# Optimization experiments

Hardware: AMD Instinct MI355X
Metric: run time of the kernel (lower is better)

Reference implementation:

```python
import jax, jax.numpy as jnp
import numpy as np

DIM = 768
HEAD = 12


def setup_inputs() -> dict:
    key = jax.random.key(0)
    ks = jax.random.split(key, 7)
    B, N, C = 4, 2048, DIM
    s = 0.02
    return {
        "x": jax.random.normal(ks[0], (B, N, C), dtype=jnp.float32),
        "wq": jax.random.normal(ks[1], (C, C), dtype=jnp.float32) * s,
        "bq": jax.random.normal(ks[2], (C,), dtype=jnp.float32) * s,
        "wkv": jax.random.normal(ks[3], (C, 2 * C), dtype=jnp.float32) * s,
        "bkv": jax.random.normal(ks[4], (2 * C,), dtype=jnp.float32) * s,
        "wp": jax.random.normal(ks[5], (C, C), dtype=jnp.float32) * s,
        "bp": jax.random.normal(ks[6], (C,), dtype=jnp.float32) * s,
    }


def reference(x, wq, bq, wkv, bkv, wp, bp):
    B, N, C = x.shape
    H = HEAD
    D = C // H
    scale = D ** -0.5
    # projections
    q = (x @ wq + bq).reshape(B, N, H, D)          # [B,N,H,D]
    kv = (x @ wkv + bkv).reshape(B, N, 2, H, D)
    k = kv[:, :, 0]                                 # [B,N,H,D]
    v = kv[:, :, 1]
    # attention scores [B,H,N,N]
    attn = jnp.einsum('bnhd,bmhd->bhnm', q, k) * scale
    attn = jax.nn.softmax(attn, axis=-1)
    x_atten = jnp.einsum('bhnm,bmhd->bnhd', attn, v).reshape(B, N, C)
    return x_atten @ wp + bp
```

## Files before the change

kernel.cpp:

```cpp
#include <hip/hip_runtime.h>

typedef unsigned short u16;
typedef __attribute__((ext_vector_type(8))) short bf16x8;
typedef __attribute__((ext_vector_type(4))) float f32x4;

#define MFMA(a, b, c) __builtin_amdgcn_mfma_f32_16x16x32_bf16(a, b, c, 0, 0, 0)
#define LOG2E 1.44269504088896340736f

__device__ __forceinline__ u16 f2bf(float f) {
    union { float f; unsigned u; } v; v.f = f;
    unsigned r = v.u + 0x7fffu + ((v.u >> 16) & 1u);
    return (u16)(r >> 16);
}
__device__ __forceinline__ float bf2f(u16 h) {
    union { unsigned u; float f; } v; v.u = ((unsigned)h) << 16;
    return v.f;
}
__device__ __forceinline__ unsigned pkbf(float a, float b) {
#if __has_builtin(__builtin_amdgcn_cvt_pk_bf16_f32)
    typedef __attribute__((ext_vector_type(2))) __bf16 bf2_t;
    bf2_t v = __builtin_amdgcn_cvt_pk_bf16_f32(a, b);
    return __builtin_bit_cast(unsigned, v);
#else
    return (unsigned)f2bf(a) | ((unsigned)f2bf(b) << 16);
#endif
}
__device__ __forceinline__ float ex2(float x) {
#if __has_builtin(__builtin_amdgcn_exp2f)
    return __builtin_amdgcn_exp2f(x);
#else
    return exp2f(x);
#endif
}
__device__ __forceinline__ bf16x8 frag_from(unsigned a, unsigned b, unsigned c, unsigned d) {
    uint4 v; v.x = a; v.y = b; v.z = c; v.w = d;
    return __builtin_bit_cast(bf16x8, v);
}

__device__ __forceinline__ void g2l16(const void* g, void* lds_base) {
    __builtin_amdgcn_global_load_lds(
        (const __attribute__((address_space(1))) unsigned*)(unsigned long long)(uintptr_t)g,
        (__attribute__((address_space(3))) unsigned*)(unsigned)(uintptr_t)lds_base,
        16, 0, 0);
}

__global__ __launch_bounds__(256) void prep_kernel(
    const float* __restrict__ x, const float* __restrict__ wq,
    const float* __restrict__ wkv, const float* __restrict__ wp,
    u16* __restrict__ xb, u16* __restrict__ wtqkv, u16* __restrict__ wtp)
{
    int bz = blockIdx.x;
    int t = threadIdx.x;
    if (bz < 6144) {
        int i = (bz * 256 + t) * 4;
        float4 v = *(const float4*)&x[i];
        uint2 o;
        o.x = pkbf(v.x, v.y);
        o.y = pkbf(v.z, v.w);
        *(uint2*)&xb[i] = o;
        return;
    }
    __shared__ float tile[32][33];
    const float* W; u16* Wt; int cols; int r = bz - 6144;
    if (r < 576)       { W = wq;  Wt = wtqkv;             cols = 768;  }
    else if (r < 1728) { W = wkv; Wt = wtqkv + 768 * 768; cols = 1536; r -= 576; }
    else               { W = wp;  Wt = wtp;               cols = 768;  r -= 1728; }
    int nbx = cols / 32;
    int bx = (r % nbx) * 32, by = (r / nbx) * 32;
    int tx = t & 31, ty = t >> 5;
    for (int i = 0; i < 4; i++)
        tile[ty + 8 * i][tx] = W[(size_t)(by + ty + 8 * i) * cols + bx + tx];
    __syncthreads();
    for (int i = 0; i < 4; i++)
        Wt[(size_t)(bx + ty + 8 * i) * 768 + by + tx] = f2bf(tile[tx][ty + 8 * i]);
}

__global__ __launch_bounds__(256, 3) void gemm128(
    const u16* __restrict__ A, const u16* __restrict__ Bt,
    const float* __restrict__ bias0, const float* __restrict__ bias1, int bsplit,
    u16* __restrict__ outB, u16* __restrict__ vtg, int M, int N, int K)
{
    __shared__ __align__(16) u16 smem[17408];
    u16* As = smem;
    u16* Bs = smem + 8192;
    u16* Cs = smem;

    int t = threadIdx.x;
    int w = t >> 6, l = t & 63, q4 = l >> 4, lm = l & 15, lm7 = l & 7;
    int bm = blockIdx.y * 128, bn = blockIdx.x * 128;
    int wm = (w >> 1) * 64, wn = (w & 1) * 64;

    f32x4 acc[4][4];
    for (int i = 0; i < 4; i++) for (int j = 0; j < 4; j++) acc[i][j] = (f32x4){0, 0, 0, 0};

    int srow = l >> 3;
    int schunk = (l & 7) ^ srow;

    for (int kt = 0; kt < K; kt += 64) {
        for (int p = 0; p < 4; p++) {
            int row = p * 32 + w * 8 + srow;
            g2l16(&A [(size_t)(bm + row) * K + kt + schunk * 8], &As[(p * 32 + w * 8) * 64]);
            g2l16(&Bt[(size_t)(bn + row) * K + kt + schunk * 8], &Bs[(p * 32 + w * 8) * 64]);
        }
        __syncthreads();
        bf16x8 a[4][2], b[4][2];
        for (int i = 0; i < 4; i++)
            for (int kc = 0; kc < 2; kc++) {
                a[i][kc] = *(const bf16x8*)&As[(wm + 16 * i + lm) * 64 + ((4 * kc + q4) ^ lm7) * 8];
                b[i][kc] = *(const bf16x8*)&Bs[(wn + 16 * i + lm) * 64 + ((4 * kc + q4) ^ lm7) * 8];
            }
        for (int kc = 0; kc < 2; kc++)
            for (int i = 0; i < 4; i++)
                for (int j = 0; j < 4; j++)
                    acc[i][j] = MFMA(a[i][kc], b[j][kc], acc[i][j]);
        __syncthreads();
    }

    for (int i = 0; i < 4; i++)
        for (int j = 0; j < 4; j++) {
            int col = bn + wn + 16 * j + lm;
            float bv = (col < bsplit) ? bias0[col] : bias1[col - bsplit];
            for (int r = 0; r < 4; r++)
                Cs[(wm + 16 * i + 4 * q4 + r) * 132 + wn + 16 * j + lm] =
                    f2bf(acc[i][j][r] + bv);
        }
    __syncthreads();

    if (bn < 1536) {
        int row = t >> 1, c0 = (t & 1) * 8;
        for (int s = 0; s < 8; s++)
            *(uint4*)&outB[(size_t)(bm + row) * N + bn + c0 + s * 16] =
                *(const uint4*)&Cs[row * 132 + c0 + s * 16];
    } else {
        int c = t >> 1, half = t & 1;
        int d = c & 63, hloc = c >> 6;
        int b = bm >> 11;
        int bh = b * 12 + ((bn - 1536) >> 6) + hloc;
        size_t rowoff = ((size_t)bh * 64 + d) * 2048 + (bm & 2047) + half * 64;
        const u16* base = &Cs[c];
        for (int oct = 0; oct < 8; oct++) {
            int n0 = 32 * (2 * half + (oct >> 2)) + 4 * (oct & 3);
            uint4 o;
            o.x = base[(n0 + 0)  * 132] | ((unsigned)base[(n0 + 1)  * 132] << 16);
            o.y = base[(n0 + 2)  * 132] | ((unsigned)base[(n0 + 3)  * 132] << 16);
            o.z = base[(n0 + 16) * 132] | ((unsigned)base[(n0 + 17) * 132] << 16);
            o.w = base[(n0 + 18) * 132] | ((unsigned)base[(n0 + 19) * 132] << 16);
            *(uint4*)&vtg[rowoff + oct * 8] = o;
        }
    }
}

__global__ __launch_bounds__(256, 4) void gemm_n64(
    const u16* __restrict__ A, const u16* __restrict__ Bt,
    const float* __restrict__ bias, float* __restrict__ outF, int M, int N, int K)
{
    __shared__ __align__(16) u16 smem[12288];
    u16* As = smem;
    u16* Bs = smem + 8192;

    int t = threadIdx.x;
    int w = t >> 6, l = t & 63, q4 = l >> 4, lm = l & 15, lm7 = l & 7;
    int bm = blockIdx.y * 128, bn = blockIdx.x * 64;
    int wm = (w >> 1) * 64, wn = (w & 1) * 32;

    f32x4 acc[4][2];
    for (int i = 0; i < 4; i++) for (int j = 0; j < 2; j++) acc[i][j] = (f32x4){0, 0, 0, 0};

    int srow = l >> 3;
    int schunk = (l & 7) ^ srow;

    for (int kt = 0; kt < K; kt += 64) {
        for (int p = 0; p < 4; p++) {
            int row = p * 32 + w * 8 + srow;
            g2l16(&A[(size_t)(bm + row) * K + kt + schunk * 8], &As[(p * 32 + w * 8) * 64]);
        }
        for (int p = 0; p < 2; p++) {
            int row = p * 32 + w * 8 + srow;
            g2l16(&Bt[(size_t)(bn + row) * K + kt + schunk * 8], &Bs[(p * 32 + w * 8) * 64]);
        }
        __syncthreads();
        bf16x8 a[4][2], b[2][2];
        for (int i = 0; i < 4; i++)
            for (int kc = 0; kc < 2; kc++)
                a[i][kc] = *(const bf16x8*)&As[(wm + 16 * i + lm) * 64 + ((4 * kc + q4) ^ lm7) * 8];
        for (int j = 0; j < 2; j++)
            for (int kc = 0; kc < 2; kc++)
                b[j][kc] = *(const bf16x8*)&Bs[(wn + 16 * j + lm) * 64 + ((4 * kc + q4) ^ lm7) * 8];
        for (int kc = 0; kc < 2; kc++)
            for (int i = 0; i < 4; i++)
                for (int j = 0; j < 2; j++)
                    acc[i][j] = MFMA(a[i][kc], b[j][kc], acc[i][j]);
        __syncthreads();
    }

    for (int i = 0; i < 4; i++)
        for (int j = 0; j < 2; j++) {
            int col = bn + wn + 16 * j + lm;
            float bv = bias[col];
            for (int r = 0; r < 4; r++) {
                int row = bm + wm + 16 * i + 4 * q4 + r;
                outF[(size_t)row * N + col] = acc[i][j][r] + bv;
            }
        }
}

__global__ __launch_bounds__(256, 3) void attn_kernel(const u16* __restrict__ qkv,
                                                      const u16* __restrict__ vtg,
                                                      u16* __restrict__ xatt)
{
    __shared__ __align__(16) u16 smem[16384];

    int t = threadIdx.x;
    int w = t >> 6, l = t & 63, q4 = l >> 4, lm = l & 15, lm7 = l & 7;
    int h = blockIdx.y, b = blockIdx.z;
    int qw = blockIdx.x * 128 + w * 32;
    size_t rowbase = (size_t)b * 2048;
    int bh = b * 12 + h;

    int srow = l >> 3;
    int schunk = (l & 7) ^ srow;
    const u16* ksrc[2];
    const u16* vsrc[2];
    for (int p = 0; p < 2; p++) {
        int row = w * 16 + p * 8 + srow;
        ksrc[p] = &qkv[(rowbase + row) * 2304 + 768 + h * 64 + schunk * 8];
        vsrc[p] = &vtg[((size_t)bh * 64 + row) * 2048 + schunk * 8];
    }

    bf16x8 qf[2][2];
    for (int qi = 0; qi < 2; qi++) {
        size_t row = rowbase + qw + 16 * qi + lm;
        for (int kq = 0; kq < 2; kq++) {
            bf16x8 raw = *(const bf16x8*)&qkv[row * 2304 + h * 64 + kq * 32 + q4 * 8];
            bf16x8 sc;
            for (int j = 0; j < 8; j++) sc[j] = (short)f2bf(bf2f((u16)raw[j]) * (0.125f * LOG2E));
            qf[qi][kq] = sc;
        }
    }

    int offA = lm * 64 + (q4 ^ lm7) * 8;
    int offB = lm * 64 + ((4 | q4) ^ lm7) * 8;

    float lst[2] = {0.f, 0.f};
    f32x4 acc[2][4];
    for (int qi = 0; qi < 2; qi++)
        for (int dt = 0; dt < 4; dt++) acc[qi][dt] = (f32x4){0, 0, 0, 0};

    for (int p = 0; p < 2; p++) {
        g2l16(ksrc[p], smem + (w * 16 + p * 8) * 64);
        g2l16(vsrc[p], smem + 8192 + (w * 16 + p * 8) * 64);
    }

    for (int it = 0; it < 32; it++) {
        __syncthreads();
        int buf = it & 1;
        if (it + 1 < 32) {
            int nbuf = buf ^ 1;
            for (int p = 0; p < 2; p++) {
                g2l16(ksrc[p] + (size_t)(it + 1) * 64 * 2304,
                      smem + nbuf * 4096 + (w * 16 + p * 8) * 64);
                g2l16(vsrc[p] + (it + 1) * 64,
                      smem + 8192 + nbuf * 4096 + (w * 16 + p * 8) * 64);
            }
        }
        const u16* Kb = smem + buf * 4096;
        const u16* Vb = smem + 8192 + buf * 4096;

        f32x4 s[2][4];
        for (int kt2 = 0; kt2 < 4; kt2++) {
            bf16x8 kf0 = *(const bf16x8*)&Kb[kt2 * 1024 + offA];
            bf16x8 kf1 = *(const bf16x8*)&Kb[kt2 * 1024 + offB];
            for (int qi = 0; qi < 2; qi++) {
                f32x4 z = {0, 0, 0, 0};
                z = MFMA(kf0, qf[qi][0], z);
                z = MFMA(kf1, qf[qi][1], z);
                s[qi][kt2] = z;
            }
        }

        bf16x8 vf0[4], vf1[4];
        for (int dt = 0; dt < 4; dt++) {
            vf0[dt] = *(const bf16x8*)&Vb[dt * 1024 + offA];
            vf1[dt] = *(const bf16x8*)&Vb[dt * 1024 + offB];
        }

        for (int qi = 0; qi < 2; qi++) {
            float su = 0.f;
            uint2 pk[4];
            for (int kt2 = 0; kt2 < 4; kt2++) {
                float p0 = ex2(s[qi][kt2][0]);
                float p1 = ex2(s[qi][kt2][1]);
                float p2 = ex2(s[qi][kt2][2]);
                float p3 = ex2(s[qi][kt2][3]);
                su += (p0 + p1) + (p2 + p3);
                pk[kt2].x = pkbf(p0, p1);
                pk[kt2].y = pkbf(p2, p3);
            }
            su += __shfl_xor(su, 16);
            su += __shfl_xor(su, 32);
            lst[qi] += su;

            bf16x8 af0 = frag_from(pk[0].x, pk[0].y, pk[1].x, pk[1].y);
            bf16x8 af1 = frag_from(pk[2].x, pk[2].y, pk[3].x, pk[3].y);
            for (int dt = 0; dt < 4; dt++) {
                acc[qi][dt] = MFMA(af0, vf0[dt], acc[qi][dt]);
                acc[qi][dt] = MFMA(af1, vf1[dt], acc[qi][dt]);
            }
        }
    }

    for (int qi = 0; qi < 2; qi++) {
        float linv = 1.0f / lst[qi];
        float ar[4];
        for (int r = 0; r < 4; r++) ar[r] = __shfl(linv, 4 * q4 + r);
        for (int dt = 0; dt < 4; dt++)
            for (int r = 0; r < 4; r++) {
                int row = qw + 16 * qi + 4 * q4 + r;
                xatt[(rowbase + row) * 768 + h * 64 + 16 * dt + lm] =
                    f2bf(acc[qi][dt][r] * ar[r]);
            }
    }
}

extern "C" void kernel_launch(void* const* d_in, const int* in_sizes, int n_in,
                              void* d_out, int out_size, void* d_ws, size_t ws_size,
                              hipStream_t stream)
{
    const float* x   = (const float*)d_in[0];
    const float* wq  = (const float*)d_in[1];
    const float* bq  = (const float*)d_in[2];
    const float* wkv = (const float*)d_in[3];
    const float* bkv = (const float*)d_in[4];
    const float* wp  = (const float*)d_in[5];
    const float* bp  = (const float*)d_in[6];
    float* out = (float*)d_out;

    char* ws = (char*)d_ws;
    u16* xb    = (u16*)(ws);
    u16* wtqkv = (u16*)(ws + 12582912);
    u16* wtp   = (u16*)(ws + 16121856);
    u16* qkvb  = (u16*)(ws + 17301504);
    u16* xatt  = (u16*)(ws + 55050240);
    u16* vtg   = (u16*)(ws + 67632128);

    prep_kernel<<<8448, 256, 0, stream>>>(x, wq, wkv, wp, xb, wtqkv, wtp);

    gemm128<<<dim3(2304 / 128, 8192 / 128), 256, 0, stream>>>(
        xb, wtqkv, bq, bkv, 768, qkvb, vtg, 8192, 2304, 768);

    attn_kernel<<<dim3(16, 12, 4), 256, 0, stream>>>(qkvb, vtg, xatt);

    gemm_n64<<<dim3(768 / 64, 8192 / 128), 256, 0, stream>>>(
        xatt, wtp, bp, out, 8192, 768, 768);
}
```

Measured before the change: 221.6 us.

## Cut register pressure in GEMMs, defer softmax row-sum reduction, remap attention grid

The GEMM kernels now load A/B fragments one k-chunk at a time, which lowers live registers, and gemm128's launch bounds rise to 4 waves per SIMD. The V-transpose epilogue writes packed column-major values into shared memory and reads them back as vector loads instead of gathering scalars. In attention, the cross-lane shuffle reduction of the row sum moves out of the inner loop to the end, and the grid is flattened so consecutive blocks cover different batch-heads. Higher occupancy may cause spills, and the new block order changes how K/V data is shared in cache.

New measurement: 211.9 us. 4.4% less time.

```diff
diff --git a/kernel.cpp b/kernel.cpp
--- a/kernel.cpp
+++ b/kernel.cpp
@@ -75,7 +75,7 @@
         Wt[(size_t)(bx + ty + 8 * i) * 768 + by + tx] = f2bf(tile[tx][ty + 8 * i]);
 }
 
-__global__ __launch_bounds__(256, 3) void gemm128(
+__global__ __launch_bounds__(256, 4) void gemm128(
     const u16* __restrict__ A, const u16* __restrict__ Bt,
     const float* __restrict__ bias0, const float* __restrict__ bias1, int bsplit,
     u16* __restrict__ outB, u16* __restrict__ vtg, int M, int N, int K)
@@ -103,48 +103,55 @@
             g2l16(&Bt[(size_t)(bn + row) * K + kt + schunk * 8], &Bs[(p * 32 + w * 8) * 64]);
         }
         __syncthreads();
-        bf16x8 a[4][2], b[4][2];
-        for (int i = 0; i < 4; i++)
-            for (int kc = 0; kc < 2; kc++) {
-                a[i][kc] = *(const bf16x8*)&As[(wm + 16 * i + lm) * 64 + ((4 * kc + q4) ^ lm7) * 8];
-                b[i][kc] = *(const bf16x8*)&Bs[(wn + 16 * i + lm) * 64 + ((4 * kc + q4) ^ lm7) * 8];
-            }
-        for (int kc = 0; kc < 2; kc++)
+        for (int kc = 0; kc < 2; kc++) {
+            bf16x8 a[4], b[4];
+            for (int i = 0; i < 4; i++)
+                a[i] = *(const bf16x8*)&As[(wm + 16 * i + lm) * 64 + ((4 * kc + q4) ^ lm7) * 8];
+            for (int j = 0; j < 4; j++)
+                b[j] = *(const bf16x8*)&Bs[(wn + 16 * j + lm) * 64 + ((4 * kc + q4) ^ lm7) * 8];
             for (int i = 0; i < 4; i++)
                 for (int j = 0; j < 4; j++)
-                    acc[i][j] = MFMA(a[i][kc], b[j][kc], acc[i][j]);
-        __syncthreads();
-    }
-
-    for (int i = 0; i < 4; i++)
-        for (int j = 0; j < 4; j++) {
-            int col = bn + wn + 16 * j + lm;
-            float bv = (col < bsplit) ? bias0[col] : bias1[col - bsplit];
-            for (int r = 0; r < 4; r++)
-                Cs[(wm + 16 * i + 4 * q4 + r) * 132 + wn + 16 * j + lm] =
-                    f2bf(acc[i][j][r] + bv);
-        }
-    __syncthreads();
+                    acc[i][j] = MFMA(a[i], b[j], acc[i][j]);
+        }
+        __syncthreads();
+    }
 
     if (bn < 1536) {
+        for (int i = 0; i < 4; i++)
+            for (int j = 0; j < 4; j++) {
+                int col = bn + wn + 16 * j + lm;
+                float bv = (col < bsplit) ? bias0[col] : bias1[col - bsplit];
+                for (int r = 0; r < 4; r++)
+                    Cs[(wm + 16 * i + 4 * q4 + r) * 132 + wn + 16 * j + lm] =
+                        f2bf(acc[i][j][r] + bv);
+            }
+        __syncthreads();
         int row = t >> 1, c0 = (t & 1) * 8;
         for (int s = 0; s < 8; s++)
             *(uint4*)&outB[(size_t)(bm + row) * N + bn + c0 + s * 16] =
                 *(const uint4*)&Cs[row * 132 + c0 + s * 16];
     } else {
+        for (int i = 0; i < 4; i++)
+            for (int j = 0; j < 4; j++) {
+                int cl = wn + 16 * j + lm;
+                float bv = bias1[bn + cl - bsplit];
+                uint2 pk;
+                pk.x = pkbf(acc[i][j][0] + bv, acc[i][j][1] + bv);
+                pk.y = pkbf(acc[i][j][2] + bv, acc[i][j][3] + bv);
+                *(uint2*)&Cs[cl * 132 + wm + 16 * i + 4 * q4] = pk;
+            }
+        __syncthreads();
         int c = t >> 1, half = t & 1;
         int d = c & 63, hloc = c >> 6;
         int b = bm >> 11;
         int bh = b * 12 + ((bn - 1536) >> 6) + hloc;
         size_t rowoff = ((size_t)bh * 64 + d) * 2048 + (bm & 2047) + half * 64;
-        const u16* base = &Cs[c];
+        const u16* base = &Cs[c * 132 + half * 64];
         for (int oct = 0; oct < 8; oct++) {
-            int n0 = 32 * (2 * half + (oct >> 2)) + 4 * (oct & 3);
-            uint4 o;
-            o.x = base[(n0 + 0)  * 132] | ((unsigned)base[(n0 + 1)  * 132] << 16);
-            o.y = base[(n0 + 2)  * 132] | ((unsigned)base[(n0 + 3)  * 132] << 16);
-            o.z = base[(n0 + 16) * 132] | ((unsigned)base[(n0 + 17) * 132] << 16);
-            o.w = base[(n0 + 18) * 132] | ((unsigned)base[(n0 + 19) * 132] << 16);
+            int n0 = 32 * (oct >> 2) + 4 * (oct & 3);
+            uint2 lo = *(const uint2*)&base[n0];
+            uint2 hi = *(const uint2*)&base[n0 + 16];
+            uint4 o; o.x = lo.x; o.y = lo.y; o.z = hi.x; o.w = hi.y;
             *(uint4*)&vtg[rowoff + oct * 8] = o;
         }
     }
@@ -179,17 +186,16 @@
             g2l16(&Bt[(size_t)(bn + row) * K + kt + schunk * 8], &Bs[(p * 32 + w * 8) * 64]);
         }
         __syncthreads();
-        bf16x8 a[4][2], b[2][2];
-        for (int i = 0; i < 4; i++)
-            for (int kc = 0; kc < 2; kc++)
-                a[i][kc] = *(const bf16x8*)&As[(wm + 16 * i + lm) * 64 + ((4 * kc + q4) ^ lm7) * 8];
-        for (int j = 0; j < 2; j++)
-            for (int kc = 0; kc < 2; kc++)
-                b[j][kc] = *(const bf16x8*)&Bs[(wn + 16 * j + lm) * 64 + ((4 * kc + q4) ^ lm7) * 8];
-        for (int kc = 0; kc < 2; kc++)
+        for (int kc = 0; kc < 2; kc++) {
+            bf16x8 a[4], b[2];
+            for (int i = 0; i < 4; i++)
+                a[i] = *(const bf16x8*)&As[(wm + 16 * i + lm) * 64 + ((4 * kc + q4) ^ lm7) * 8];
+            for (int j = 0; j < 2; j++)
+                b[j] = *(const bf16x8*)&Bs[(wn + 16 * j + lm) * 64 + ((4 * kc + q4) ^ lm7) * 8];
             for (int i = 0; i < 4; i++)
                 for (int j = 0; j < 2; j++)
-                    acc[i][j] = MFMA(a[i][kc], b[j][kc], acc[i][j]);
+                    acc[i][j] = MFMA(a[i], b[j], acc[i][j]);
+        }
         __syncthreads();
     }
 
@@ -210,21 +216,23 @@
 {
     __shared__ __align__(16) u16 smem[16384];
 
+    int gid = blockIdx.x;
+    int bh = gid % 48, qt = gid / 48;
+    int b = bh / 12, h = bh % 12;
+
     int t = threadIdx.x;
     int w = t >> 6, l = t & 63, q4 = l >> 4, lm = l & 15, lm7 = l & 7;
-    int h = blockIdx.y, b = blockIdx.z;
-    int qw = blockIdx.x * 128 + w * 32;
+    int qw = qt * 128 + w * 32;
     size_t rowbase = (size_t)b * 2048;
-    int bh = b * 12 + h;
 
     int srow = l >> 3;
     int schunk = (l & 7) ^ srow;
-    const u16* ksrc[2];
-    const u16* vsrc[2];
+    const u16* kp[2];
+    const u16* vp[2];
     for (int p = 0; p < 2; p++) {
         int row = w * 16 + p * 8 + srow;
-        ksrc[p] = &qkv[(rowbase + row) * 2304 + 768 + h * 64 + schunk * 8];
-        vsrc[p] = &vtg[((size_t)bh * 64 + row) * 2048 + schunk * 8];
+        kp[p] = &qkv[(rowbase + row) * 2304 + 768 + h * 64 + schunk * 8];
+        vp[p] = &vtg[((size_t)bh * 64 + row) * 2048 + schunk * 8];
     }
 
     bf16x8 qf[2][2];
@@ -247,20 +255,21 @@
         for (int dt = 0; dt < 4; dt++) acc[qi][dt] = (f32x4){0, 0, 0, 0};
 
     for (int p = 0; p < 2; p++) {
-        g2l16(ksrc[p], smem + (w * 16 + p * 8) * 64);
-        g2l16(vsrc[p], smem + 8192 + (w * 16 + p * 8) * 64);
-    }
-
+        g2l16(kp[p], smem + (w * 16 + p * 8) * 64);
+        g2l16(vp[p], smem + 8192 + (w * 16 + p * 8) * 64);
+    }
+
+    const size_t KSTEP = (size_t)64 * 2304;
     for (int it = 0; it < 32; it++) {
         __syncthreads();
         int buf = it & 1;
         if (it + 1 < 32) {
             int nbuf = buf ^ 1;
             for (int p = 0; p < 2; p++) {
-                g2l16(ksrc[p] + (size_t)(it + 1) * 64 * 2304,
-                      smem + nbuf * 4096 + (w * 16 + p * 8) * 64);
-                g2l16(vsrc[p] + (it + 1) * 64,
-                      smem + 8192 + nbuf * 4096 + (w * 16 + p * 8) * 64);
+                kp[p] += KSTEP;
+                vp[p] += 64;
+                g2l16(kp[p], smem + nbuf * 4096 + (w * 16 + p * 8) * 64);
+                g2l16(vp[p], smem + 8192 + nbuf * 4096 + (w * 16 + p * 8) * 64);
             }
         }
         const u16* Kb = smem + buf * 4096;
@@ -296,8 +305,6 @@
                 pk[kt2].x = pkbf(p0, p1);
                 pk[kt2].y = pkbf(p2, p3);
             }
-            su += __shfl_xor(su, 16);
-            su += __shfl_xor(su, 32);
             lst[qi] += su;
 
             bf16x8 af0 = frag_from(pk[0].x, pk[0].y, pk[1].x, pk[1].y);
@@ -310,7 +317,10 @@
     }
 
     for (int qi = 0; qi < 2; qi++) {
-        float linv = 1.0f / lst[qi];
+        float su = lst[qi];
+        su += __shfl_xor(su, 16);
+        su += __shfl_xor(su, 32);
+        float linv = 1.0f / su;
         float ar[4];
         for (int r = 0; r < 4; r++) ar[r] = __shfl(linv, 4 * q4 + r);
         for (int dt = 0; dt < 4; dt++)
@@ -348,7 +358,7 @@
     gemm128<<<dim3(2304 / 128, 8192 / 128), 256, 0, stream>>>(
         xb, wtqkv, bq, bkv, 768, qkvb, vtg, 8192, 2304, 768);
 
-    attn_kernel<<<dim3(16, 12, 4), 256, 0, stream>>>(qkvb, vtg, xatt);
+    attn_kernel<<<768, 256, 0, stream>>>(qkvb, vtg, xatt);
 
     gemm_n64<<<dim3(768 / 64, 8192 / 128), 256, 0, stream>>>(
         xatt, wtp, bp, out, 8192, 768, 768);
```
